# Optimization experiments

Measured on AMD Instinct MI355X. Metric: run time of the kernel, lower is better.

Reference implementation:

```python
import jax, jax.numpy as jnp
import numpy as np

N, B, D, Q = 32, 36, 2048, 1024  # batch, objects, v_dim, q_dim


def setup_inputs() -> dict:
    key = jax.random.key(0)
    ks = jax.random.split(key, 6)
    sc = 0.02  # small init so ReLU chains stay well-scaled
    return {
        "v": jax.random.normal(ks[0], (N, B, D), jnp.float32),
        "q": jax.random.normal(ks[1], (N, Q), jnp.float32),
        "W1": jax.random.normal(ks[2], (D, D), jnp.float32) * sc,
        "b1": jnp.zeros((D,), jnp.float32),
        "W2": jax.random.normal(ks[3], (D, D), jnp.float32) * sc,
        "b2": jnp.zeros((D,), jnp.float32),
        "W3": jax.random.normal(ks[4], (Q, D), jnp.float32) * sc,
        "b3": jnp.zeros((D,), jnp.float32),
    }


def reference(v, q, W1, b1, W2, b2, W3, b3):
    # FCNet = ReLU(Linear(.)) with weight-norm folded, dropout=0 (eval).
    # Original calls linear3 twice (linear4 unused bug), so q_emb == q_emb2.
    qe = jax.nn.relu(q @ W3 + b3)  # (N, D)
    # pairs[n,i,j] = v[n,i]*qe[n] + v[n,j]*qe[n]  -> (N, B, B, D)
    pairs = (v[:, :, None, :] + v[:, None, :, :]) * qe[:, None, None, :]
    h = jax.nn.relu(jnp.einsum('nijd,de->nije', pairs, W1) + b1)  # linear1
    x = jnp.sum(h, axis=2)  # sum over j relations -> (N, B, D)
    return jax.nn.relu(x @ W2 + b2)  # linear2
```

## Files before the change

kernel.cpp:

```cpp
#include <hip/hip_runtime.h>
#include <stdint.h>

#define N_BATCH 32
#define B_OBJ   36
#define D_DIM   2048
#define Q_DIM   1024

typedef __bf16 bf16x8 __attribute__((ext_vector_type(8)));
typedef float  f32x4  __attribute__((ext_vector_type(4)));

__device__ __forceinline__ uint16_t f2bf(float f) {
    uint32_t u = __builtin_bit_cast(uint32_t, f);
    uint32_t r = (u + 0x7FFFu + ((u >> 16) & 1u)) >> 16;
    return (uint16_t)r;
}

__device__ __forceinline__ void gld_lds16(const void* g, void* l) {
    __builtin_amdgcn_global_load_lds(
        (const __attribute__((address_space(1))) uint32_t*)g,
        (__attribute__((address_space(3))) uint32_t*)l, 16, 0, 0);
}

__global__ __launch_bounds__(256) void transpose_all(
    const float* __restrict__ W1, const float* __restrict__ W2,
    const float* __restrict__ W3,
    uint16_t* __restrict__ W1t, uint16_t* __restrict__ W2t,
    uint16_t* __restrict__ W3t) {
    __shared__ float tile[64][65];
    int gy = blockIdx.y;
    const float* W; uint16_t* Wt; int K, k0;
    if (gy < 32)      { W = W1; Wt = W1t; K = 2048; k0 = gy * 64; }
    else if (gy < 64) { W = W2; Wt = W2t; K = 2048; k0 = (gy - 32) * 64; }
    else              { W = W3; Wt = W3t; K = 1024; k0 = (gy - 64) * 64; }
    int n0 = blockIdx.x * 64;
    int t = threadIdx.x;
    {
        int r = t >> 4, c = (t & 15) * 4;
#pragma unroll
        for (int p = 0; p < 4; ++p)
            *(float4*)&tile[r + p * 16][c] =
                *(const float4*)&W[(size_t)(k0 + r + p * 16) * 2048 + n0 + c];
    }
    __syncthreads();
    {
        int n = t >> 2, kb = (t & 3) * 16;
#pragma unroll
        for (int g4 = 0; g4 < 4; ++g4) {
            int k = kb + g4 * 4;
            ushort4 o;
            o.x = f2bf(tile[k][n]);     o.y = f2bf(tile[k + 1][n]);
            o.z = f2bf(tile[k + 2][n]); o.w = f2bf(tile[k + 3][n]);
            *(ushort4*)&Wt[(size_t)(n0 + n) * K + k0 + k] = o;
        }
    }
}

__global__ __launch_bounds__(256) void qk_gemm(
    const float* __restrict__ q,
    const uint16_t* __restrict__ W3t,
    float* __restrict__ qpart) {
    __shared__ __align__(16) uint16_t As[32][32];
    __shared__ __align__(16) uint16_t Bs[128][32];
    int t = threadIdx.x, lane = t & 63, wave = t >> 6;
    int l15 = lane & 15, quad = lane >> 4;
    int n0 = blockIdx.x * 128;
    int kbase = blockIdx.y * 256;
    f32x4 acc[2][2] = {};
    int ar = t >> 3, ac = (t & 7) * 4;
    int br = t >> 2, bk = (t & 3) * 8;

    for (int k0 = 0; k0 < 256; k0 += 32) {
        __syncthreads();
        float4 av = *(const float4*)&q[(size_t)ar * Q_DIM + kbase + k0 + ac];
        ushort4 a4;
        a4.x = f2bf(av.x); a4.y = f2bf(av.y); a4.z = f2bf(av.z); a4.w = f2bf(av.w);
        *(ushort4*)&As[ar][ac] = a4;
        *(uint4*)&Bs[br][bk]      = *(const uint4*)&W3t[(size_t)(n0 + br) * Q_DIM + kbase + k0 + bk];
        *(uint4*)&Bs[br + 64][bk] = *(const uint4*)&W3t[(size_t)(n0 + br + 64) * Q_DIM + kbase + k0 + bk];
        __syncthreads();
        bf16x8 af[2], bfr[2];
        af[0]  = *(const bf16x8*)&As[l15][quad * 8];
        af[1]  = *(const bf16x8*)&As[16 + l15][quad * 8];
        bfr[0] = *(const bf16x8*)&Bs[wave * 32 + l15][quad * 8];
        bfr[1] = *(const bf16x8*)&Bs[wave * 32 + 16 + l15][quad * 8];
#pragma unroll
        for (int i = 0; i < 2; ++i)
#pragma unroll
            for (int j = 0; j < 2; ++j)
                acc[i][j] = __builtin_amdgcn_mfma_f32_16x16x32_bf16(af[i], bfr[j], acc[i][j], 0, 0, 0);
    }
    float* dst = qpart + (size_t)blockIdx.y * 32 * D_DIM;
#pragma unroll
    for (int i = 0; i < 2; ++i)
#pragma unroll
        for (int j = 0; j < 2; ++j) {
            int n = n0 + wave * 32 + j * 16 + l15;
#pragma unroll
            for (int r = 0; r < 4; ++r)
                dst[(size_t)(i * 16 + quad * 4 + r) * D_DIM + n] = acc[i][j][r];
        }
}

__global__ __launch_bounds__(128) void qe_make_u(
    const float* __restrict__ qpart, const float* __restrict__ b3,
    const float* __restrict__ v, uint16_t* __restrict__ u) {
    int nb = blockIdx.z;
    int og = blockIdx.y;
    int d4 = blockIdx.x * 128 + threadIdx.x;
    const float4* p = (const float4*)qpart;
    size_t base = (size_t)nb * 512 + d4;
    float4 s0 = p[base], s1 = p[16384 + base], s2 = p[32768 + base], s3 = p[49152 + base];
    float4 b = ((const float4*)b3)[d4];
    float4 qe;
    qe.x = fmaxf(s0.x + s1.x + s2.x + s3.x + b.x, 0.f);
    qe.y = fmaxf(s0.y + s1.y + s2.y + s3.y + b.y, 0.f);
    qe.z = fmaxf(s0.z + s1.z + s2.z + s3.z + b.z, 0.f);
    qe.w = fmaxf(s0.w + s1.w + s2.w + s3.w + b.w, 0.f);
    const float4* v4 = (const float4*)v;
    ushort4* u4 = (ushort4*)u;
    size_t rb = (size_t)nb * B_OBJ * 512 + d4 + (size_t)og * 6 * 512;
#pragma unroll
    for (int i = 0; i < 6; ++i) {
        float4 vv = v4[rb + (size_t)i * 512];
        ushort4 o;
        o.x = f2bf(vv.x * qe.x);
        o.y = f2bf(vv.y * qe.y);
        o.z = f2bf(vv.z * qe.z);
        o.w = f2bf(vv.w * qe.w);
        u4[rb + (size_t)i * 512] = o;
    }
}

__global__ __launch_bounds__(512) void gemm_batch(
    const uint16_t* __restrict__ A,
    const uint16_t* __restrict__ Bt,
    const float* __restrict__ bias,
    void* __restrict__ Cv,
    int mode) {
    extern __shared__ __align__(16) uint16_t smem[];
    float* yt = (float*)smem;

    int t = threadIdx.x, lane = t & 63, wave = t >> 6;
    int l15 = lane & 15, quad = lane >> 4;
    int wr = wave >> 2, wc = wave & 3;
    int nbp = blockIdx.y;
    int n0 = blockIdx.x * 128;
    const uint16_t* Ab = A + (size_t)nbp * 72 * D_DIM;

    const uint16_t* gp[7];
    int loff[7];
    int wslot = (lane & 3) ^ ((lane >> 2) & 3);
#pragma unroll
    for (int c = 0; c < 7; ++c) {
        int r = wave + 8 * c;
        if (r < 24) {
            int g = r >> 2, h = r & 3;
            int arow = g * 16 + (lane >> 2) - (g >= 3 ? 12 : 0);
            gp[c] = Ab + (size_t)arow * D_DIM + h * 32 + wslot * 8;
            loff[c] = h * 3072 + g * 512;
        } else {
            int rb = r - 24, g = rb >> 2, h = rb & 3;
            int brow = g * 16 + (lane >> 2);
            gp[c] = Bt + (size_t)(n0 + brow) * D_DIM + h * 32 + wslot * 8;
            loff[c] = 12288 + h * 4096 + g * 512;
        }
    }

    f32x4 acc[3][2] = {};
    int rslot = quad ^ (l15 & 3);

#define STAGE(kk, bi)                                            \
    {                                                            \
        _Pragma("unroll")                                        \
        for (int c = 0; c < 7; ++c)                              \
            gld_lds16(gp[c] + (kk), smem + (bi) * 28672 + loff[c]); \
    }

    STAGE(0, 0);
    STAGE(128, 1);
    asm volatile("s_waitcnt vmcnt(7)" ::: "memory");
    __builtin_amdgcn_s_barrier();

    for (int k = 0; k < 16; ++k) {
        int cur = k & 1;
        const uint16_t* As = smem + cur * 28672;
        const uint16_t* Bs = As + 12288;
#pragma unroll
        for (int s = 0; s < 4; ++s) {
            bf16x8 af[3], bfr[2];
#pragma unroll
            for (int i = 0; i < 3; ++i)
                af[i] = *(const bf16x8*)(As + s * 3072 + (wr * 48 + i * 16 + l15) * 32 + rslot * 8);
#pragma unroll
            for (int j = 0; j < 2; ++j)
                bfr[j] = *(const bf16x8*)(Bs + s * 4096 + (wc * 32 + j * 16 + l15) * 32 + rslot * 8);
#pragma unroll
            for (int i = 0; i < 3; ++i)
#pragma unroll
                for (int j = 0; j < 2; ++j)
                    acc[i][j] = __builtin_amdgcn_mfma_f32_16x16x32_bf16(af[i], bfr[j], acc[i][j], 0, 0, 0);
        }
        if (k == 15) break;
        __builtin_amdgcn_s_barrier();
        if (k < 14) {
            STAGE((k + 2) * 128, cur);
            asm volatile("s_waitcnt vmcnt(7)" ::: "memory");
        } else {
            asm volatile("s_waitcnt vmcnt(0)" ::: "memory");
        }
        __builtin_amdgcn_s_barrier();
    }
#undef STAGE

    if (mode == 0) {
        uint16_t* X = (uint16_t*)Cv;
        __syncthreads();
#pragma unroll
        for (int i = 0; i < 3; ++i)
#pragma unroll
            for (int j = 0; j < 2; ++j)
#pragma unroll
                for (int r = 0; r < 4; ++r)
                    yt[(wr * 48 + i * 16 + quad * 4 + r) * 132 + wc * 32 + j * 16 + l15] = acc[i][j][r];
        __syncthreads();
        int col = t & 127, sub = t >> 7;
        int b = sub >> 1, half = sub & 1;
        float bv = bias[n0 + col];
        float z[36];
#pragma unroll
        for (int j = 0; j < 36; ++j) z[j] = yt[(b * 48 + j) * 132 + col];
#pragma unroll
        for (int ii = 0; ii < 18; ++ii) {
            int i = half * 18 + ii;
            float zi = z[i] + bv;
            float s = 0.f;
#pragma unroll
            for (int j = 0; j < 36; ++j) s += fmaxf(zi + z[j], 0.f);
            X[(size_t)((nbp * 2 + b) * B_OBJ + i) * D_DIM + n0 + col] = f2bf(s);
        }
    } else {
        float* O = (float*)Cv;
#pragma unroll
        for (int i = 0; i < 3; ++i)
#pragma unroll
            for (int r = 0; r < 4; ++r) {
                int obj = i * 16 + quad * 4 + r;
                if (obj < B_OBJ) {
#pragma unroll
                    for (int j = 0; j < 2; ++j) {
                        int cc = n0 + wc * 32 + j * 16 + l15;
                        O[(size_t)((nbp * 2 + wr) * B_OBJ + obj) * D_DIM + cc] =
                            fmaxf(acc[i][j][r] + bias[cc], 0.f);
                    }
                }
            }
    }
}

extern "C" void kernel_launch(void* const* d_in, const int* in_sizes, int n_in,
                              void* d_out, int out_size, void* d_ws, size_t ws_size,
                              hipStream_t stream) {
    const float* v  = (const float*)d_in[0];
    const float* q  = (const float*)d_in[1];
    const float* W1 = (const float*)d_in[2];
    const float* b1 = (const float*)d_in[3];
    const float* W2 = (const float*)d_in[4];
    const float* b2 = (const float*)d_in[5];
    const float* W3 = (const float*)d_in[6];
    const float* b3 = (const float*)d_in[7];
    float* out = (float*)d_out;

    char* ws = (char*)d_ws;
    uint16_t* W1t   = (uint16_t*)(ws + 0);
    uint16_t* W2t   = (uint16_t*)(ws + 8388608);
    uint16_t* W3t   = (uint16_t*)(ws + 16777216);
    uint16_t* u     = (uint16_t*)(ws + 16777216);
    float*    qpart = (float*)   (ws + 21495808);
    uint16_t* x     = (uint16_t*)(ws + 22806528);

    static bool attr_done = false;
    if (!attr_done) {
        (void)hipFuncSetAttribute((const void*)gemm_batch,
                                  hipFuncAttributeMaxDynamicSharedMemorySize, 114688);
        attr_done = true;
    }

    transpose_all<<<dim3(32, 80), 256, 0, stream>>>(W1, W2, W3, W1t, W2t, W3t);

    qk_gemm<<<dim3(16, 4), 256, 0, stream>>>(q, W3t, qpart);

    qe_make_u<<<dim3(4, 6, N_BATCH), 128, 0, stream>>>(qpart, b3, v, u);

    gemm_batch<<<dim3(16, 16), 512, 114688, stream>>>(u, W1t, b1, x, 0);

    gemm_batch<<<dim3(16, 16), 512, 114688, stream>>>(x, W2t, b2, out, 1);
}
```

Baseline: 164.3 us.

## Read fp32 W3 directly in q-GEMM and widen split-K to 16 chunks

Stops transposing and converting W3 to bf16 in the weight-prep kernel. The q@W3 GEMM now loads fp32 W3 rows straight into shared memory and converts them to bf16 fragments when building the MFMA operands. Split-K grows from 4 to 16 chunks, so 256 blocks launch instead of 64, and the reduction kernel sums 16 partial slices. This removes a transpose pass and its round trip through the workspace, at the cost of more partial-sum traffic and strided shared-memory reads during conversion.

```diff
diff --git a/kernel.cpp b/kernel.cpp
--- a/kernel.cpp
+++ b/kernel.cpp
@@ -8,6 +8,7 @@
 
 typedef __bf16 bf16x8 __attribute__((ext_vector_type(8)));
 typedef float  f32x4  __attribute__((ext_vector_type(4)));
+typedef uint16_t u16x8 __attribute__((ext_vector_type(8)));
 
 __device__ __forceinline__ uint16_t f2bf(float f) {
     uint32_t u = __builtin_bit_cast(uint32_t, f);
@@ -23,15 +24,12 @@
 
 __global__ __launch_bounds__(256) void transpose_all(
     const float* __restrict__ W1, const float* __restrict__ W2,
-    const float* __restrict__ W3,
-    uint16_t* __restrict__ W1t, uint16_t* __restrict__ W2t,
-    uint16_t* __restrict__ W3t) {
+    uint16_t* __restrict__ W1t, uint16_t* __restrict__ W2t) {
     __shared__ float tile[64][65];
     int gy = blockIdx.y;
-    const float* W; uint16_t* Wt; int K, k0;
-    if (gy < 32)      { W = W1; Wt = W1t; K = 2048; k0 = gy * 64; }
-    else if (gy < 64) { W = W2; Wt = W2t; K = 2048; k0 = (gy - 32) * 64; }
-    else              { W = W3; Wt = W3t; K = 1024; k0 = (gy - 64) * 64; }
+    const float* W; uint16_t* Wt; int k0;
+    if (gy < 32) { W = W1; Wt = W1t; k0 = gy * 64; }
+    else         { W = W2; Wt = W2t; k0 = (gy - 32) * 64; }
     int n0 = blockIdx.x * 64;
     int t = threadIdx.x;
     {
@@ -50,39 +48,48 @@
             ushort4 o;
             o.x = f2bf(tile[k][n]);     o.y = f2bf(tile[k + 1][n]);
             o.z = f2bf(tile[k + 2][n]); o.w = f2bf(tile[k + 3][n]);
-            *(ushort4*)&Wt[(size_t)(n0 + n) * K + k0 + k] = o;
+            *(ushort4*)&Wt[(size_t)(n0 + n) * 2048 + k0 + k] = o;
         }
     }
 }
 
 __global__ __launch_bounds__(256) void qk_gemm(
     const float* __restrict__ q,
-    const uint16_t* __restrict__ W3t,
+    const float* __restrict__ W3,
     float* __restrict__ qpart) {
     __shared__ __align__(16) uint16_t As[32][32];
-    __shared__ __align__(16) uint16_t Bs[128][32];
+    __shared__ __align__(16) float tile[32][132];
     int t = threadIdx.x, lane = t & 63, wave = t >> 6;
     int l15 = lane & 15, quad = lane >> 4;
     int n0 = blockIdx.x * 128;
-    int kbase = blockIdx.y * 256;
+    int kbase = blockIdx.y * 64;
     f32x4 acc[2][2] = {};
     int ar = t >> 3, ac = (t & 7) * 4;
-    int br = t >> 2, bk = (t & 3) * 8;
-
-    for (int k0 = 0; k0 < 256; k0 += 32) {
+    int kr = t >> 3, nc = (t & 7) * 16;
+
+    for (int k0 = 0; k0 < 64; k0 += 32) {
         __syncthreads();
         float4 av = *(const float4*)&q[(size_t)ar * Q_DIM + kbase + k0 + ac];
         ushort4 a4;
         a4.x = f2bf(av.x); a4.y = f2bf(av.y); a4.z = f2bf(av.z); a4.w = f2bf(av.w);
         *(ushort4*)&As[ar][ac] = a4;
-        *(uint4*)&Bs[br][bk]      = *(const uint4*)&W3t[(size_t)(n0 + br) * Q_DIM + kbase + k0 + bk];
-        *(uint4*)&Bs[br + 64][bk] = *(const uint4*)&W3t[(size_t)(n0 + br + 64) * Q_DIM + kbase + k0 + bk];
+        const float* wrow = &W3[(size_t)(kbase + k0 + kr) * 2048 + n0 + nc];
+#pragma unroll
+        for (int g = 0; g < 4; ++g)
+            *(float4*)&tile[kr][nc + g * 4] = *(const float4*)(wrow + g * 4);
         __syncthreads();
         bf16x8 af[2], bfr[2];
-        af[0]  = *(const bf16x8*)&As[l15][quad * 8];
-        af[1]  = *(const bf16x8*)&As[16 + l15][quad * 8];
-        bfr[0] = *(const bf16x8*)&Bs[wave * 32 + l15][quad * 8];
-        bfr[1] = *(const bf16x8*)&Bs[wave * 32 + 16 + l15][quad * 8];
+        af[0] = *(const bf16x8*)&As[l15][quad * 8];
+        af[1] = *(const bf16x8*)&As[16 + l15][quad * 8];
+#pragma unroll
+        for (int j = 0; j < 2; ++j) {
+            int n = wave * 32 + j * 16 + l15;
+            u16x8 pk;
+#pragma unroll
+            for (int e = 0; e < 8; ++e)
+                pk[e] = f2bf(tile[quad * 8 + e][n]);
+            bfr[j] = __builtin_bit_cast(bf16x8, pk);
+        }
 #pragma unroll
         for (int i = 0; i < 2; ++i)
 #pragma unroll
@@ -109,13 +116,15 @@
     int d4 = blockIdx.x * 128 + threadIdx.x;
     const float4* p = (const float4*)qpart;
     size_t base = (size_t)nb * 512 + d4;
-    float4 s0 = p[base], s1 = p[16384 + base], s2 = p[32768 + base], s3 = p[49152 + base];
-    float4 b = ((const float4*)b3)[d4];
+    float4 a = ((const float4*)b3)[d4];
+#pragma unroll
+    for (int z = 0; z < 16; ++z) {
+        float4 s = p[(size_t)z * 16384 + base];
+        a.x += s.x; a.y += s.y; a.z += s.z; a.w += s.w;
+    }
     float4 qe;
-    qe.x = fmaxf(s0.x + s1.x + s2.x + s3.x + b.x, 0.f);
-    qe.y = fmaxf(s0.y + s1.y + s2.y + s3.y + b.y, 0.f);
-    qe.z = fmaxf(s0.z + s1.z + s2.z + s3.z + b.z, 0.f);
-    qe.w = fmaxf(s0.w + s1.w + s2.w + s3.w + b.w, 0.f);
+    qe.x = fmaxf(a.x, 0.f); qe.y = fmaxf(a.y, 0.f);
+    qe.z = fmaxf(a.z, 0.f); qe.w = fmaxf(a.w, 0.f);
     const float4* v4 = (const float4*)v;
     ushort4* u4 = (ushort4*)u;
     size_t rb = (size_t)nb * B_OBJ * 512 + d4 + (size_t)og * 6 * 512;
@@ -273,10 +282,9 @@
     char* ws = (char*)d_ws;
     uint16_t* W1t   = (uint16_t*)(ws + 0);
     uint16_t* W2t   = (uint16_t*)(ws + 8388608);
-    uint16_t* W3t   = (uint16_t*)(ws + 16777216);
     uint16_t* u     = (uint16_t*)(ws + 16777216);
     float*    qpart = (float*)   (ws + 21495808);
-    uint16_t* x     = (uint16_t*)(ws + 22806528);
+    uint16_t* x     = (uint16_t*)(ws + 25690112);
 
     static bool attr_done = false;
     if (!attr_done) {
@@ -285,9 +293,9 @@
         attr_done = true;
     }
 
-    transpose_all<<<dim3(32, 80), 256, 0, stream>>>(W1, W2, W3, W1t, W2t, W3t);
-
-    qk_gemm<<<dim3(16, 4), 256, 0, stream>>>(q, W3t, qpart);
+    transpose_all<<<dim3(32, 64), 256, 0, stream>>>(W1, W2, W1t, W2t);
+
+    qk_gemm<<<dim3(16, 16), 256, 0, stream>>>(q, W3, qpart);
 
     qe_make_u<<<dim3(4, 6, N_BATCH), 128, 0, stream>>>(qpart, b3, v, u);
 
```

Result: faster. 160.8 us (-2.2%).
